# Kernel tuning notes

Measured on AMD Instinct MI355X. Metric: run time of the kernel, lower is better.

## Reference

```python
import jax, jax.numpy as jnp
import numpy as np

E = 8       # n_experts
TOPK = 2    # n_activated_experts


def setup_inputs() -> dict:
    key = jax.random.key(0)
    ks = jax.random.split(key, 5)
    B, T, C, F = 2, 1024, 1024, 2816
    scale = 0.02
    return {
        "x": jax.random.normal(ks[0], (B, T, C), dtype=jnp.float32),
        "Wg": jax.random.normal(ks[1], (C, E), dtype=jnp.float32) * scale,
        "W1": jax.random.normal(ks[2], (E, C, F), dtype=jnp.float32) * scale,
        "W3": jax.random.normal(ks[3], (E, C, F), dtype=jnp.float32) * scale,
        "W2": jax.random.normal(ks[4], (E, F, C), dtype=jnp.float32) * scale,
    }


def reference(x, Wg, W1, W3, W2):
    B, T, C = x.shape
    xt = x.reshape(-1, C)                                  # [N, C], N = B*T
    router = xt @ Wg                                       # [N, E]
    probs, indices = jax.lax.top_k(router, TOPK)           # [N, K] each, descending like torch.topk
    probs = jax.nn.softmax(probs.astype(jnp.float32), axis=1).astype(x.dtype)
    # combine[n, e] = sum_k probs[n, k] * (indices[n, k] == e)
    onehot = (indices[:, :, None] == jnp.arange(E)).astype(x.dtype)  # [N, K, E]
    combine = jnp.einsum("nk,nke->ne", probs, onehot)      # [N, E]
    # SwiGLU experts, computed densely then combined with routing weights
    h1 = jnp.einsum("nc,ecf->enf", xt, W1)                 # [E, N, F]
    h3 = jnp.einsum("nc,ecf->enf", xt, W3)                 # [E, N, F]
    h = jax.nn.silu(h1) * h3                               # [E, N, F]
    yexp = jnp.einsum("enf,efc->enc", h, W2)               # [E, N, C]
    y = jnp.einsum("ne,enc->nc", combine, yexp)            # [N, C]
    return (y.reshape(B, T, C), indices)
```

## Files before the change

### kernel.cpp

```cpp
#include <hip/hip_runtime.h>
#include <hip/hip_bf16.h>

#define NE 8
#define C 1024
#define F 2816
#define LDK 40

typedef __bf16 bf16_t;
typedef bf16_t bf16x8 __attribute__((ext_vector_type(8)));
typedef float f32x4 __attribute__((ext_vector_type(4)));

__device__ inline unsigned pk2(float a, float b) {
    union { bf16_t h[2]; unsigned u; } x;
    x.h[0] = (bf16_t)a; x.h[1] = (bf16_t)b;
    return x.u;
}

__global__ void router_kernel(const float* __restrict__ x, const float* __restrict__ Wg,
                              float* __restrict__ probs, int* __restrict__ idxbuf,
                              float* __restrict__ out_idx) {
    const int n = blockIdx.x;
    const int lane = threadIdx.x;
    const float* xr = x + (size_t)n * C;
    float acc[NE] = {0.f, 0.f, 0.f, 0.f, 0.f, 0.f, 0.f, 0.f};
    #pragma unroll
    for (int i = 0; i < C / 64; i++) {
        int c = i * 64 + lane;
        float xv = xr[c];
        const float4* w = (const float4*)(Wg + (size_t)c * NE);
        float4 w0 = w[0], w1 = w[1];
        acc[0] += xv * w0.x; acc[1] += xv * w0.y; acc[2] += xv * w0.z; acc[3] += xv * w0.w;
        acc[4] += xv * w1.x; acc[5] += xv * w1.y; acc[6] += xv * w1.z; acc[7] += xv * w1.w;
    }
    #pragma unroll
    for (int off = 32; off >= 1; off >>= 1)
        #pragma unroll
        for (int e = 0; e < NE; e++) acc[e] += __shfl_down(acc[e], off);
    if (lane == 0) {
        float v0 = -1e30f, v1 = -1e30f; int i0 = 0, i1 = 0;
        #pragma unroll
        for (int e = 0; e < NE; e++) {
            float v = acc[e];
            if (v > v0)      { v1 = v0; i1 = i0; v0 = v; i0 = e; }
            else if (v > v1) { v1 = v; i1 = e; }
        }
        float e1 = __expf(v1 - v0);
        float p0 = 1.0f / (1.0f + e1);
        probs[n * 2]     = p0;
        probs[n * 2 + 1] = e1 / (1.0f + e1);
        idxbuf[n * 2]     = i0;
        idxbuf[n * 2 + 1] = i1;
        out_idx[n * 2]     = (float)i0;
        out_idx[n * 2 + 1] = (float)i1;
    }
}

__global__ void group_kernel(const int* __restrict__ idxbuf, int* __restrict__ rowinfo,
                             int* __restrict__ counts, int* __restrict__ offs, int N) {
    __shared__ int cnt[NE], run[NE], base[NE];
    const int t = threadIdx.x;
    if (t < NE) { cnt[t] = 0; run[t] = 0; }
    __syncthreads();
    for (int i = t; i < N * 2; i += blockDim.x) atomicAdd(&cnt[idxbuf[i]], 1);
    __syncthreads();
    if (t == 0) { int s = 0; for (int e = 0; e < NE; e++) { base[e] = s; s += cnt[e]; } }
    __syncthreads();
    for (int i = t; i < N * 2; i += blockDim.x) {
        int e = idxbuf[i];
        int p = atomicAdd(&run[e], 1);
        rowinfo[base[e] + p] = i;
    }
    if (t < NE) { counts[t] = cnt[t]; offs[t] = base[t]; }
}

__global__ __launch_bounds__(256, 2)
void gemm1_kernel(const float* __restrict__ x, const float* __restrict__ W1,
                  const float* __restrict__ W3, const int* __restrict__ rowinfo,
                  const int* __restrict__ counts, const int* __restrict__ offs,
                  bf16_t* __restrict__ hbuf) {
    const int e = blockIdx.z;
    const int cnt = counts[e];
    const int m0 = blockIdx.y * 128;
    if (m0 >= cnt) return;
    const int base = offs[e];
    const int f0 = blockIdx.x * 128;
    const int t = threadIdx.x;
    const int lane = t & 63, wave = t >> 6;
    const int wm = (wave >> 1) * 64, wn = (wave & 1) * 64;
    const int lr = lane & 15, quad = lane >> 4;

    __shared__ __align__(16) bf16_t As[128 * LDK];
    __shared__ __align__(16) bf16_t B1s[128 * LDK];
    __shared__ __align__(16) bf16_t B3s[128 * LDK];

    const int am = t >> 1;
    const int ak = (t & 1) * 16;
    const int tok = rowinfo[base + min(m0 + am, cnt - 1)] >> 1;
    const float* aptr = x + (size_t)tok * C + ak;

    const int bf = t & 127;
    const int bk0 = (t >> 7) * 8;
    const float* b1ptr = W1 + (size_t)e * C * F + f0 + bf;
    const float* b3ptr = W3 + (size_t)e * C * F + f0 + bf;

    f32x4 acc1[4][4], acc3[4][4];
    const f32x4 zero = {0.f, 0.f, 0.f, 0.f};
    #pragma unroll
    for (int im = 0; im < 4; im++)
        #pragma unroll
        for (int in = 0; in < 4; in++) { acc1[im][in] = zero; acc3[im][in] = zero; }

    for (int kc = 0; kc < C; kc += 32) {
        const float4* ap = (const float4*)(aptr + kc);
        float4 a0 = ap[0], a1 = ap[1], a2 = ap[2], a3 = ap[3];
        uint4 av0 = make_uint4(pk2(a0.x, a0.y), pk2(a0.z, a0.w), pk2(a1.x, a1.y), pk2(a1.z, a1.w));
        uint4 av1 = make_uint4(pk2(a2.x, a2.y), pk2(a2.z, a2.w), pk2(a3.x, a3.y), pk2(a3.z, a3.w));
        *(uint4*)(&As[am * LDK + ak])     = av0;
        *(uint4*)(&As[am * LDK + ak + 8]) = av1;
        #pragma unroll
        for (int g = 0; g < 2; g++) {
            const int kk = kc + bk0 + g * 16;
            const float* p1 = b1ptr + (size_t)kk * F;
            float v[8];
            #pragma unroll
            for (int i = 0; i < 8; i++) v[i] = p1[(size_t)i * F];
            uint4 bv1 = make_uint4(pk2(v[0], v[1]), pk2(v[2], v[3]), pk2(v[4], v[5]), pk2(v[6], v[7]));
            *(uint4*)(&B1s[bf * LDK + bk0 + g * 16]) = bv1;
            const float* p3 = b3ptr + (size_t)kk * F;
            #pragma unroll
            for (int i = 0; i < 8; i++) v[i] = p3[(size_t)i * F];
            uint4 bv3 = make_uint4(pk2(v[0], v[1]), pk2(v[2], v[3]), pk2(v[4], v[5]), pk2(v[6], v[7]));
            *(uint4*)(&B3s[bf * LDK + bk0 + g * 16]) = bv3;
        }
        __syncthreads();
        bf16x8 af[4], b1f[4], b3f[4];
        #pragma unroll
        for (int im = 0; im < 4; im++)
            af[im] = *(const bf16x8*)(&As[(wm + im * 16 + lr) * LDK + quad * 8]);
        #pragma unroll
        for (int in = 0; in < 4; in++) {
            b1f[in] = *(const bf16x8*)(&B1s[(wn + in * 16 + lr) * LDK + quad * 8]);
            b3f[in] = *(const bf16x8*)(&B3s[(wn + in * 16 + lr) * LDK + quad * 8]);
        }
        #pragma unroll
        for (int im = 0; im < 4; im++)
            #pragma unroll
            for (int in = 0; in < 4; in++) {
                acc1[im][in] = __builtin_amdgcn_mfma_f32_16x16x32_bf16(af[im], b1f[in], acc1[im][in], 0, 0, 0);
                acc3[im][in] = __builtin_amdgcn_mfma_f32_16x16x32_bf16(af[im], b3f[in], acc3[im][in], 0, 0, 0);
            }
        __syncthreads();
    }
    #pragma unroll
    for (int im = 0; im < 4; im++) {
        #pragma unroll
        for (int r = 0; r < 4; r++) {
            const int row = wm + im * 16 + quad * 4 + r;
            const int gi = m0 + row;
            if (gi < cnt) {
                bf16_t* hp = hbuf + (size_t)(base + gi) * F + f0 + wn + lr;
                #pragma unroll
                for (int in = 0; in < 4; in++) {
                    float h1 = acc1[im][in][r], h3 = acc3[im][in][r];
                    float s = h1 / (1.0f + __expf(-h1)) * h3;
                    hp[in * 16] = (bf16_t)s;
                }
            }
        }
    }
}

__global__ __launch_bounds__(256, 2)
void gemm2_kernel(const bf16_t* __restrict__ hbuf, const float* __restrict__ W2,
                  const int* __restrict__ rowinfo, const int* __restrict__ counts,
                  const int* __restrict__ offs, float* __restrict__ contrib) {
    const int e = blockIdx.z;
    const int cnt = counts[e];
    const int m0 = blockIdx.y * 128;
    if (m0 >= cnt) return;
    const int base = offs[e];
    const int c0 = blockIdx.x * 128;
    const int t = threadIdx.x;
    const int lane = t & 63, wave = t >> 6;
    const int wm = (wave >> 1) * 64, wn = (wave & 1) * 64;
    const int lr = lane & 15, quad = lane >> 4;

    __shared__ __align__(16) bf16_t As[128 * LDK];
    __shared__ __align__(16) bf16_t Bs[128 * LDK];

    const int am = t >> 1;
    const int ak = (t & 1) * 16;
    const bf16_t* aptr = hbuf + (size_t)(base + min(m0 + am, cnt - 1)) * F + ak;

    const int bfc = t & 127;
    const int bk0 = (t >> 7) * 8;
    const float* bptr = W2 + (size_t)e * F * C + c0 + bfc;

    f32x4 acc[4][4];
    const f32x4 zero = {0.f, 0.f, 0.f, 0.f};
    #pragma unroll
    for (int im = 0; im < 4; im++)
        #pragma unroll
        for (int in = 0; in < 4; in++) acc[im][in] = zero;

    for (int kc = 0; kc < F; kc += 32) {
        const uint4* ap = (const uint4*)(aptr + kc);
        *(uint4*)(&As[am * LDK + ak])     = ap[0];
        *(uint4*)(&As[am * LDK + ak + 8]) = ap[1];
        #pragma unroll
        for (int g = 0; g < 2; g++) {
            const int kk = kc + bk0 + g * 16;
            const float* p = bptr + (size_t)kk * C;
            float v[8];
            #pragma unroll
            for (int i = 0; i < 8; i++) v[i] = p[(size_t)i * C];
            uint4 bv = make_uint4(pk2(v[0], v[1]), pk2(v[2], v[3]), pk2(v[4], v[5]), pk2(v[6], v[7]));
            *(uint4*)(&Bs[bfc * LDK + bk0 + g * 16]) = bv;
        }
        __syncthreads();
        bf16x8 af[4], bf_[4];
        #pragma unroll
        for (int im = 0; im < 4; im++)
            af[im] = *(const bf16x8*)(&As[(wm + im * 16 + lr) * LDK + quad * 8]);
        #pragma unroll
        for (int in = 0; in < 4; in++)
            bf_[in] = *(const bf16x8*)(&Bs[(wn + in * 16 + lr) * LDK + quad * 8]);
        #pragma unroll
        for (int im = 0; im < 4; im++)
            #pragma unroll
            for (int in = 0; in < 4; in++)
                acc[im][in] = __builtin_amdgcn_mfma_f32_16x16x32_bf16(af[im], bf_[in], acc[im][in], 0, 0, 0);
        __syncthreads();
    }
    #pragma unroll
    for (int im = 0; im < 4; im++) {
        #pragma unroll
        for (int r = 0; r < 4; r++) {
            const int row = wm + im * 16 + quad * 4 + r;
            const int gi = m0 + row;
            if (gi < cnt) {
                const int slot = rowinfo[base + gi];
                float* cp = contrib + (size_t)slot * C + c0 + wn + lr;
                #pragma unroll
                for (int in = 0; in < 4; in++) cp[in * 16] = acc[im][in][r];
            }
        }
    }
}

__global__ void combine_kernel(const float* __restrict__ contrib, const float* __restrict__ probs,
                               float* __restrict__ y) {
    const int idx = blockIdx.x * blockDim.x + threadIdx.x;
    const int n = idx >> 8;
    const int c = (idx & 255) * 4;
    const float p0 = probs[n * 2], p1 = probs[n * 2 + 1];
    const float4 a = *(const float4*)(contrib + ((size_t)n * 2) * C + c);
    const float4 b = *(const float4*)(contrib + ((size_t)n * 2 + 1) * C + c);
    float4 o;
    o.x = p0 * a.x + p1 * b.x;
    o.y = p0 * a.y + p1 * b.y;
    o.z = p0 * a.z + p1 * b.z;
    o.w = p0 * a.w + p1 * b.w;
    *(float4*)(y + (size_t)n * C + c) = o;
}

extern "C" void kernel_launch(void* const* d_in, const int* in_sizes, int n_in,
                              void* d_out, int out_size, void* d_ws, size_t ws_size,
                              hipStream_t stream) {
    const float* x  = (const float*)d_in[0];
    const float* Wg = (const float*)d_in[1];
    const float* W1 = (const float*)d_in[2];
    const float* W3 = (const float*)d_in[3];
    const float* W2 = (const float*)d_in[4];
    const int N = in_sizes[0] / C;

    float* y = (float*)d_out;
    float* out_idx = y + (size_t)N * C;

    char* ws = (char*)d_ws;
    float* probs  = (float*)ws;
    int* idxbuf   = (int*)(ws + (size_t)N * 2 * 4);
    int* rowinfo  = (int*)(ws + (size_t)N * 4 * 4);
    int* counts   = (int*)(ws + (size_t)N * 6 * 4);
    int* offs     = (int*)(ws + (size_t)N * 6 * 4 + 64);
    size_t hoff = ((size_t)N * 6 * 4 + 1024 + 255) & ~(size_t)255;
    bf16_t* hbuf = (bf16_t*)(ws + hoff);
    size_t coff = (hoff + (size_t)N * 2 * F * 2 + 255) & ~(size_t)255;
    float* contrib = (float*)(ws + coff);

    const int mtiles = (N + 127) / 128;

    router_kernel<<<N, 64, 0, stream>>>(x, Wg, probs, idxbuf, out_idx);
    group_kernel<<<1, 256, 0, stream>>>(idxbuf, rowinfo, counts, offs, N);
    gemm1_kernel<<<dim3(F / 128, mtiles, NE), 256, 0, stream>>>(x, W1, W3, rowinfo, counts, offs, hbuf);
    gemm2_kernel<<<dim3(C / 128, mtiles, NE), 256, 0, stream>>>(hbuf, W2, rowinfo, counts, offs, contrib);
    combine_kernel<<<(N * C / 4 + 255) / 256, 256, 0, stream>>>(contrib, probs, y);
}
```

Measured before the change: 525.9 us.

## Pre-convert weights to transposed bf16, async LDS loads, split-K second GEMM

Adds a kernel that converts W1/W3/W2 to bf16 and transposes them to K-contiguous layout each call. Activations are also written to bf16 inside the router kernel. Both GEMMs now load tiles with global_load_lds direct-to-LDS 16-byte copies instead of strided fp32 loads plus register conversion. The second GEMM uses split-K with partial buffers and a reduction kernel. The per-call weight conversion costs an extra full read of the fp32 weights and a write of the bf16 copies. The unpadded LDS layout may add bank conflicts.

```diff
diff --git a/kernel.cpp b/kernel.cpp
--- a/kernel.cpp
+++ b/kernel.cpp
@@ -4,7 +4,6 @@
 #define NE 8
 #define C 1024
 #define F 2816
-#define LDK 40
 
 typedef __bf16 bf16_t;
 typedef bf16_t bf16x8 __attribute__((ext_vector_type(8)));
@@ -16,17 +15,25 @@
     return x.u;
 }
 
+__device__ __forceinline__ void async_ld16(const bf16_t* g, bf16_t* l) {
+    __builtin_amdgcn_global_load_lds(
+        (const __attribute__((address_space(1))) unsigned int*)g,
+        (__attribute__((address_space(3))) unsigned int*)l, 16, 0, 0);
+}
+
 __global__ void router_kernel(const float* __restrict__ x, const float* __restrict__ Wg,
                               float* __restrict__ probs, int* __restrict__ idxbuf,
-                              float* __restrict__ out_idx) {
+                              float* __restrict__ out_idx, bf16_t* __restrict__ xb) {
     const int n = blockIdx.x;
     const int lane = threadIdx.x;
     const float* xr = x + (size_t)n * C;
+    bf16_t* xbr = xb + (size_t)n * C;
     float acc[NE] = {0.f, 0.f, 0.f, 0.f, 0.f, 0.f, 0.f, 0.f};
     #pragma unroll
     for (int i = 0; i < C / 64; i++) {
         int c = i * 64 + lane;
         float xv = xr[c];
+        xbr[c] = (bf16_t)xv;
         const float4* w = (const float4*)(Wg + (size_t)c * NE);
         float4 w0 = w[0], w1 = w[1];
         acc[0] += xv * w0.x; acc[1] += xv * w0.y; acc[2] += xv * w0.z; acc[3] += xv * w0.w;
@@ -45,8 +52,7 @@
             else if (v > v1) { v1 = v; i1 = e; }
         }
         float e1 = __expf(v1 - v0);
-        float p0 = 1.0f / (1.0f + e1);
-        probs[n * 2]     = p0;
+        probs[n * 2]     = 1.0f / (1.0f + e1);
         probs[n * 2 + 1] = e1 / (1.0f + e1);
         idxbuf[n * 2]     = i0;
         idxbuf[n * 2 + 1] = i1;
@@ -73,35 +79,80 @@
     if (t < NE) { counts[t] = cnt[t]; offs[t] = base[t]; }
 }
 
+__global__ __launch_bounds__(256)
+void convert_kernel(const float* __restrict__ W1, const float* __restrict__ W3,
+                    const float* __restrict__ W2, bf16_t* __restrict__ Wt1,
+                    bf16_t* __restrict__ Wt3, bf16_t* __restrict__ Wt2) {
+    const int yy = blockIdx.y;
+    const int which = yy >> 3, e = yy & 7;
+    const float* src; bf16_t* dst; int R, Cc;
+    if (which == 0)      { src = W1; dst = Wt1; R = C; Cc = F; }
+    else if (which == 1) { src = W3; dst = Wt3; R = C; Cc = F; }
+    else                 { src = W2; dst = Wt2; R = F; Cc = C; }
+    src += (size_t)e * C * F;
+    dst += (size_t)e * C * F;
+    const int tiles_r = R >> 6;
+    const int bx = blockIdx.x;
+    const int tr = bx % tiles_r, tc = bx / tiles_r;
+    const int t = threadIdx.x;
+    __shared__ __align__(16) bf16_t tile[64 * 72];
+
+    const int mr = t >> 4, mc = t & 15;
+    const float* sp = src + (size_t)(tr * 64 + mr * 4) * Cc + tc * 64 + mc * 4;
+    float4 v0 = *(const float4*)(sp);
+    float4 v1 = *(const float4*)(sp + Cc);
+    float4 v2 = *(const float4*)(sp + 2 * (size_t)Cc);
+    float4 v3 = *(const float4*)(sp + 3 * (size_t)Cc);
+    uint2 u;
+    u.x = pk2(v0.x, v1.x); u.y = pk2(v2.x, v3.x); *(uint2*)&tile[(mc * 4 + 0) * 72 + mr * 4] = u;
+    u.x = pk2(v0.y, v1.y); u.y = pk2(v2.y, v3.y); *(uint2*)&tile[(mc * 4 + 1) * 72 + mr * 4] = u;
+    u.x = pk2(v0.z, v1.z); u.y = pk2(v2.z, v3.z); *(uint2*)&tile[(mc * 4 + 2) * 72 + mr * 4] = u;
+    u.x = pk2(v0.w, v1.w); u.y = pk2(v2.w, v3.w); *(uint2*)&tile[(mc * 4 + 3) * 72 + mr * 4] = u;
+    __syncthreads();
+    const int dc = t >> 2, rc = (t & 3) * 16;
+    uint4 o0 = *(uint4*)&tile[dc * 72 + rc];
+    uint4 o1 = *(uint4*)&tile[dc * 72 + rc + 8];
+    bf16_t* dp = dst + (size_t)(tc * 64 + dc) * R + tr * 64 + rc;
+    *(uint4*)(dp)     = o0;
+    *(uint4*)(dp + 8) = o1;
+}
+
 __global__ __launch_bounds__(256, 2)
-void gemm1_kernel(const float* __restrict__ x, const float* __restrict__ W1,
-                  const float* __restrict__ W3, const int* __restrict__ rowinfo,
+void gemm1_kernel(const bf16_t* __restrict__ xb, const bf16_t* __restrict__ Wt1,
+                  const bf16_t* __restrict__ Wt3, const int* __restrict__ rowinfo,
                   const int* __restrict__ counts, const int* __restrict__ offs,
                   bf16_t* __restrict__ hbuf) {
     const int e = blockIdx.z;
     const int cnt = counts[e];
-    const int m0 = blockIdx.y * 128;
+    const int m0 = blockIdx.y << 7;
     if (m0 >= cnt) return;
     const int base = offs[e];
-    const int f0 = blockIdx.x * 128;
+    const int f0 = blockIdx.x << 7;
     const int t = threadIdx.x;
-    const int lane = t & 63, wave = t >> 6;
-    const int wm = (wave >> 1) * 64, wn = (wave & 1) * 64;
+    const int lane = t & 63, w = t >> 6;
     const int lr = lane & 15, quad = lane >> 4;
-
-    __shared__ __align__(16) bf16_t As[128 * LDK];
-    __shared__ __align__(16) bf16_t B1s[128 * LDK];
-    __shared__ __align__(16) bf16_t B3s[128 * LDK];
-
-    const int am = t >> 1;
-    const int ak = (t & 1) * 16;
-    const int tok = rowinfo[base + min(m0 + am, cnt - 1)] >> 1;
-    const float* aptr = x + (size_t)tok * C + ak;
-
-    const int bf = t & 127;
-    const int bk0 = (t >> 7) * 8;
-    const float* b1ptr = W1 + (size_t)e * C * F + f0 + bf;
-    const float* b3ptr = W3 + (size_t)e * C * F + f0 + bf;
+    const int wm = (w >> 1) << 6, wn = (w & 1) << 6;
+
+    __shared__ __align__(16) bf16_t As[128 * 32];
+    __shared__ __align__(16) bf16_t B1s[128 * 32];
+    __shared__ __align__(16) bf16_t B3s[128 * 32];
+
+    const int srow = w * 16 + (lane >> 2);
+    const int skoff = (lane & 3) * 8;
+    const int r0 = min(m0 + srow, cnt - 1);
+    const int r1 = min(m0 + 64 + srow, cnt - 1);
+    const bf16_t* ag0 = xb + (size_t)(rowinfo[base + r0] >> 1) * C + skoff;
+    const bf16_t* ag1 = xb + (size_t)(rowinfo[base + r1] >> 1) * C + skoff;
+    const bf16_t* b1g0 = Wt1 + ((size_t)e * F + f0 + srow) * C + skoff;
+    const bf16_t* b1g1 = b1g0 + (size_t)64 * C;
+    const bf16_t* b3g0 = Wt3 + ((size_t)e * F + f0 + srow) * C + skoff;
+    const bf16_t* b3g1 = b3g0 + (size_t)64 * C;
+    bf16_t* lA0 = &As[(w * 16) * 32];
+    bf16_t* lA1 = &As[(64 + w * 16) * 32];
+    bf16_t* lB10 = &B1s[(w * 16) * 32];
+    bf16_t* lB11 = &B1s[(64 + w * 16) * 32];
+    bf16_t* lB30 = &B3s[(w * 16) * 32];
+    bf16_t* lB31 = &B3s[(64 + w * 16) * 32];
 
     f32x4 acc1[4][4], acc3[4][4];
     const f32x4 zero = {0.f, 0.f, 0.f, 0.f};
@@ -111,36 +162,21 @@
         for (int in = 0; in < 4; in++) { acc1[im][in] = zero; acc3[im][in] = zero; }
 
     for (int kc = 0; kc < C; kc += 32) {
-        const float4* ap = (const float4*)(aptr + kc);
-        float4 a0 = ap[0], a1 = ap[1], a2 = ap[2], a3 = ap[3];
-        uint4 av0 = make_uint4(pk2(a0.x, a0.y), pk2(a0.z, a0.w), pk2(a1.x, a1.y), pk2(a1.z, a1.w));
-        uint4 av1 = make_uint4(pk2(a2.x, a2.y), pk2(a2.z, a2.w), pk2(a3.x, a3.y), pk2(a3.z, a3.w));
-        *(uint4*)(&As[am * LDK + ak])     = av0;
-        *(uint4*)(&As[am * LDK + ak + 8]) = av1;
-        #pragma unroll
-        for (int g = 0; g < 2; g++) {
-            const int kk = kc + bk0 + g * 16;
-            const float* p1 = b1ptr + (size_t)kk * F;
-            float v[8];
-            #pragma unroll
-            for (int i = 0; i < 8; i++) v[i] = p1[(size_t)i * F];
-            uint4 bv1 = make_uint4(pk2(v[0], v[1]), pk2(v[2], v[3]), pk2(v[4], v[5]), pk2(v[6], v[7]));
-            *(uint4*)(&B1s[bf * LDK + bk0 + g * 16]) = bv1;
-            const float* p3 = b3ptr + (size_t)kk * F;
-            #pragma unroll
-            for (int i = 0; i < 8; i++) v[i] = p3[(size_t)i * F];
-            uint4 bv3 = make_uint4(pk2(v[0], v[1]), pk2(v[2], v[3]), pk2(v[4], v[5]), pk2(v[6], v[7]));
-            *(uint4*)(&B3s[bf * LDK + bk0 + g * 16]) = bv3;
-        }
+        async_ld16(ag0 + kc, lA0);
+        async_ld16(ag1 + kc, lA1);
+        async_ld16(b1g0 + kc, lB10);
+        async_ld16(b1g1 + kc, lB11);
+        async_ld16(b3g0 + kc, lB30);
+        async_ld16(b3g1 + kc, lB31);
         __syncthreads();
         bf16x8 af[4], b1f[4], b3f[4];
         #pragma unroll
         for (int im = 0; im < 4; im++)
-            af[im] = *(const bf16x8*)(&As[(wm + im * 16 + lr) * LDK + quad * 8]);
+            af[im] = *(const bf16x8*)(&As[(wm + im * 16 + lr) * 32 + quad * 8]);
         #pragma unroll
         for (int in = 0; in < 4; in++) {
-            b1f[in] = *(const bf16x8*)(&B1s[(wn + in * 16 + lr) * LDK + quad * 8]);
-            b3f[in] = *(const bf16x8*)(&B3s[(wn + in * 16 + lr) * LDK + quad * 8]);
+            b1f[in] = *(const bf16x8*)(&B1s[(wn + in * 16 + lr) * 32 + quad * 8]);
+            b3f[in] = *(const bf16x8*)(&B3s[(wn + in * 16 + lr) * 32 + quad * 8]);
         }
         #pragma unroll
         for (int im = 0; im < 4; im++)
@@ -171,30 +207,40 @@
 }
 
 __global__ __launch_bounds__(256, 2)
-void gemm2_kernel(const bf16_t* __restrict__ hbuf, const float* __restrict__ W2,
+void gemm2_kernel(const bf16_t* __restrict__ hbuf, const bf16_t* __restrict__ Wt2,
                   const int* __restrict__ rowinfo, const int* __restrict__ counts,
-                  const int* __restrict__ offs, float* __restrict__ contrib) {
-    const int e = blockIdx.z;
+                  const int* __restrict__ offs, float* __restrict__ part,
+                  int PK, int nslots) {
+    const int z = blockIdx.z;
+    const int e = z & 7, ks = z >> 3;
     const int cnt = counts[e];
-    const int m0 = blockIdx.y * 128;
+    const int m0 = blockIdx.y << 7;
     if (m0 >= cnt) return;
     const int base = offs[e];
-    const int c0 = blockIdx.x * 128;
+    const int c0 = blockIdx.x << 7;
     const int t = threadIdx.x;
-    const int lane = t & 63, wave = t >> 6;
-    const int wm = (wave >> 1) * 64, wn = (wave & 1) * 64;
+    const int lane = t & 63, w = t >> 6;
     const int lr = lane & 15, quad = lane >> 4;
-
-    __shared__ __align__(16) bf16_t As[128 * LDK];
-    __shared__ __align__(16) bf16_t Bs[128 * LDK];
-
-    const int am = t >> 1;
-    const int ak = (t & 1) * 16;
-    const bf16_t* aptr = hbuf + (size_t)(base + min(m0 + am, cnt - 1)) * F + ak;
-
-    const int bfc = t & 127;
-    const int bk0 = (t >> 7) * 8;
-    const float* bptr = W2 + (size_t)e * F * C + c0 + bfc;
+    const int wm = (w >> 1) << 6, wn = (w & 1) << 6;
+
+    const int klen = F / PK;
+    const int kbeg = ks * klen, kend = kbeg + klen;
+
+    __shared__ __align__(16) bf16_t As[128 * 32];
+    __shared__ __align__(16) bf16_t Bs[128 * 32];
+
+    const int srow = w * 16 + (lane >> 2);
+    const int skoff = (lane & 3) * 8;
+    const int r0 = min(m0 + srow, cnt - 1);
+    const int r1 = min(m0 + 64 + srow, cnt - 1);
+    const bf16_t* ag0 = hbuf + (size_t)(base + r0) * F + skoff;
+    const bf16_t* ag1 = hbuf + (size_t)(base + r1) * F + skoff;
+    const bf16_t* bg0 = Wt2 + ((size_t)e * C + c0 + srow) * F + skoff;
+    const bf16_t* bg1 = bg0 + (size_t)64 * F;
+    bf16_t* lA0 = &As[(w * 16) * 32];
+    bf16_t* lA1 = &As[(64 + w * 16) * 32];
+    bf16_t* lB0 = &Bs[(w * 16) * 32];
+    bf16_t* lB1 = &Bs[(64 + w * 16) * 32];
 
     f32x4 acc[4][4];
     const f32x4 zero = {0.f, 0.f, 0.f, 0.f};
@@ -203,28 +249,19 @@
         #pragma unroll
         for (int in = 0; in < 4; in++) acc[im][in] = zero;
 
-    for (int kc = 0; kc < F; kc += 32) {
-        const uint4* ap = (const uint4*)(aptr + kc);
-        *(uint4*)(&As[am * LDK + ak])     = ap[0];
-        *(uint4*)(&As[am * LDK + ak + 8]) = ap[1];
-        #pragma unroll
-        for (int g = 0; g < 2; g++) {
-            const int kk = kc + bk0 + g * 16;
-            const float* p = bptr + (size_t)kk * C;
-            float v[8];
-            #pragma unroll
-            for (int i = 0; i < 8; i++) v[i] = p[(size_t)i * C];
-            uint4 bv = make_uint4(pk2(v[0], v[1]), pk2(v[2], v[3]), pk2(v[4], v[5]), pk2(v[6], v[7]));
-            *(uint4*)(&Bs[bfc * LDK + bk0 + g * 16]) = bv;
-        }
+    for (int kc = kbeg; kc < kend; kc += 32) {
+        async_ld16(ag0 + kc, lA0);
+        async_ld16(ag1 + kc, lA1);
+        async_ld16(bg0 + kc, lB0);
+        async_ld16(bg1 + kc, lB1);
         __syncthreads();
         bf16x8 af[4], bf_[4];
         #pragma unroll
         for (int im = 0; im < 4; im++)
-            af[im] = *(const bf16x8*)(&As[(wm + im * 16 + lr) * LDK + quad * 8]);
+            af[im] = *(const bf16x8*)(&As[(wm + im * 16 + lr) * 32 + quad * 8]);
         #pragma unroll
         for (int in = 0; in < 4; in++)
-            bf_[in] = *(const bf16x8*)(&Bs[(wn + in * 16 + lr) * LDK + quad * 8]);
+            bf_[in] = *(const bf16x8*)(&Bs[(wn + in * 16 + lr) * 32 + quad * 8]);
         #pragma unroll
         for (int im = 0; im < 4; im++)
             #pragma unroll
@@ -240,7 +277,7 @@
             const int gi = m0 + row;
             if (gi < cnt) {
                 const int slot = rowinfo[base + gi];
-                float* cp = contrib + (size_t)slot * C + c0 + wn + lr;
+                float* cp = part + ((size_t)ks * nslots + slot) * C + c0 + wn + lr;
                 #pragma unroll
                 for (int in = 0; in < 4; in++) cp[in * 16] = acc[im][in][r];
             }
@@ -248,19 +285,26 @@
     }
 }
 
-__global__ void combine_kernel(const float* __restrict__ contrib, const float* __restrict__ probs,
-                               float* __restrict__ y) {
+__global__ void reduce_kernel(const float* __restrict__ part, const float* __restrict__ probs,
+                              float* __restrict__ y, int PK, int nslots) {
     const int idx = blockIdx.x * blockDim.x + threadIdx.x;
     const int n = idx >> 8;
     const int c = (idx & 255) * 4;
+    const size_t ksstride = (size_t)nslots * C;
+    const float* b0 = part + ((size_t)n * 2) * C + c;
+    float4 s0 = {0.f, 0.f, 0.f, 0.f}, s1 = {0.f, 0.f, 0.f, 0.f};
+    for (int ks = 0; ks < PK; ks++) {
+        float4 a = *(const float4*)(b0 + ks * ksstride);
+        float4 b = *(const float4*)(b0 + ks * ksstride + C);
+        s0.x += a.x; s0.y += a.y; s0.z += a.z; s0.w += a.w;
+        s1.x += b.x; s1.y += b.y; s1.z += b.z; s1.w += b.w;
+    }
     const float p0 = probs[n * 2], p1 = probs[n * 2 + 1];
-    const float4 a = *(const float4*)(contrib + ((size_t)n * 2) * C + c);
-    const float4 b = *(const float4*)(contrib + ((size_t)n * 2 + 1) * C + c);
     float4 o;
-    o.x = p0 * a.x + p1 * b.x;
-    o.y = p0 * a.y + p1 * b.y;
-    o.z = p0 * a.z + p1 * b.z;
-    o.w = p0 * a.w + p1 * b.w;
+    o.x = p0 * s0.x + p1 * s1.x;
+    o.y = p0 * s0.y + p1 * s1.y;
+    o.z = p0 * s0.z + p1 * s1.z;
+    o.w = p0 * s0.w + p1 * s1.w;
     *(float4*)(y + (size_t)n * C + c) = o;
 }
 
@@ -273,26 +317,36 @@
     const float* W3 = (const float*)d_in[3];
     const float* W2 = (const float*)d_in[4];
     const int N = in_sizes[0] / C;
+    const int nslots = N * 2;
 
     float* y = (float*)d_out;
     float* out_idx = y + (size_t)N * C;
 
     char* ws = (char*)d_ws;
-    float* probs  = (float*)ws;
-    int* idxbuf   = (int*)(ws + (size_t)N * 2 * 4);
-    int* rowinfo  = (int*)(ws + (size_t)N * 4 * 4);
-    int* counts   = (int*)(ws + (size_t)N * 6 * 4);
-    int* offs     = (int*)(ws + (size_t)N * 6 * 4 + 64);
-    size_t hoff = ((size_t)N * 6 * 4 + 1024 + 255) & ~(size_t)255;
-    bf16_t* hbuf = (bf16_t*)(ws + hoff);
-    size_t coff = (hoff + (size_t)N * 2 * F * 2 + 255) & ~(size_t)255;
-    float* contrib = (float*)(ws + coff);
-
-    const int mtiles = (N + 127) / 128;
-
-    router_kernel<<<N, 64, 0, stream>>>(x, Wg, probs, idxbuf, out_idx);
+    size_t off = 0;
+    auto alloc = [&](size_t bytes) { size_t p = off; off = (off + bytes + 255) & ~(size_t)255; return p; };
+    float* probs   = (float*)(ws + alloc((size_t)nslots * 4));
+    int* idxbuf    = (int*)(ws + alloc((size_t)nslots * 4));
+    int* rowinfo   = (int*)(ws + alloc((size_t)nslots * 4));
+    int* counts    = (int*)(ws + alloc(64));
+    int* offs      = (int*)(ws + alloc(64));
+    bf16_t* xb     = (bf16_t*)(ws + alloc((size_t)N * C * 2));
+    bf16_t* hbuf   = (bf16_t*)(ws + alloc((size_t)nslots * F * 2));
+    bf16_t* Wt1    = (bf16_t*)(ws + alloc((size_t)NE * C * F * 2));
+    bf16_t* Wt3    = (bf16_t*)(ws + alloc((size_t)NE * C * F * 2));
+    bf16_t* Wt2    = (bf16_t*)(ws + alloc((size_t)NE * C * F * 2));
+    const size_t partbytes = (size_t)nslots * C * 4;
+    int PK = 1;
+    if (off + 4 * partbytes + 1024 <= ws_size) PK = 4;
+    else if (off + 2 * partbytes + 1024 <= ws_size) PK = 2;
+    float* part = (float*)(ws + alloc((size_t)PK * partbytes));
+
+    const int mtiles = nslots / 128;
+
+    router_kernel<<<N, 64, 0, stream>>>(x, Wg, probs, idxbuf, out_idx, xb);
     group_kernel<<<1, 256, 0, stream>>>(idxbuf, rowinfo, counts, offs, N);
-    gemm1_kernel<<<dim3(F / 128, mtiles, NE), 256, 0, stream>>>(x, W1, W3, rowinfo, counts, offs, hbuf);
-    gemm2_kernel<<<dim3(C / 128, mtiles, NE), 256, 0, stream>>>(hbuf, W2, rowinfo, counts, offs, contrib);
-    combine_kernel<<<(N * C / 4 + 255) / 256, 256, 0, stream>>>(contrib, probs, y);
-}
+    convert_kernel<<<dim3(704, 24), 256, 0, stream>>>(W1, W3, W2, Wt1, Wt3, Wt2);
+    gemm1_kernel<<<dim3(F / 128, mtiles, NE), 256, 0, stream>>>(xb, Wt1, Wt3, rowinfo, counts, offs, hbuf);
+    gemm2_kernel<<<dim3(C / 128, mtiles, NE * PK), 256, 0, stream>>>(hbuf, Wt2, rowinfo, counts, offs, part, PK, nslots);
+    reduce_kernel<<<(N * C / 4 + 255) / 256, 256, 0, stream>>>(part, probs, y, PK, nslots);
+}
```

Result: faster. 455.3 us (-13.4%).
